# Kernel optimization log

Hardware: AMD Instinct MI355X
Metric: run time of the kernel (lower is better)

Reference implementation:

```python
import jax, jax.numpy as jnp
import numpy as np

N_NODES = 100000
N_EDGES = 1600000
D_IN = 64
D_HID = 64
D_OUT = 64


def _sage_conv(x, src, dst, n_nodes, W_l, b_l, W_r):
    # mean aggregation of source features at destination nodes
    msgs = x[src]  # [E, F] gather
    agg = jax.ops.segment_sum(msgs, dst, num_segments=n_nodes)
    cnt = jax.ops.segment_sum(jnp.ones((src.shape[0],), x.dtype), dst, num_segments=n_nodes)
    mean = agg / jnp.maximum(cnt, 1.0)[:, None]  # nodes with no in-edges -> 0
    # out = lin_l(mean) + lin_r(x); lin_l has bias, lin_r does not (PyG default)
    return mean @ W_l.T + b_l + x @ W_r.T


def setup_inputs() -> dict:
    key = jax.random.key(0)
    ks = jax.random.split(key, 8)
    x = jax.random.normal(ks[0], (N_NODES, D_IN), dtype=jnp.float32)
    edge_index = jax.random.randint(ks[1], (2, N_EDGES), 0, N_NODES, dtype=jnp.int64) if jax.config.jax_enable_x64 else jax.random.randint(ks[1], (2, N_EDGES), 0, N_NODES, dtype=jnp.int32)
    s1 = 1.0 / np.sqrt(D_IN)
    s2 = 1.0 / np.sqrt(D_HID)
    W1_l = jax.random.uniform(ks[2], (D_HID, D_IN), jnp.float32, -s1, s1)
    b1_l = jax.random.uniform(ks[3], (D_HID,), jnp.float32, -s1, s1)
    W1_r = jax.random.uniform(ks[4], (D_HID, D_IN), jnp.float32, -s1, s1)
    W2_l = jax.random.uniform(ks[5], (D_OUT, D_HID), jnp.float32, -s2, s2)
    b2_l = jax.random.uniform(ks[6], (D_OUT,), jnp.float32, -s2, s2)
    W2_r = jax.random.uniform(ks[7], (D_OUT, D_HID), jnp.float32, -s2, s2)
    return {"x": x, "edge_index": edge_index, "W1_l": W1_l, "b1_l": b1_l, "W1_r": W1_r,
            "W2_l": W2_l, "b2_l": b2_l, "W2_r": W2_r}


def reference(x, edge_index, W1_l, b1_l, W1_r, W2_l, b2_l, W2_r):
    src, dst = edge_index[0], edge_index[1]
    h = _sage_conv(x, src, dst, x.shape[0], W1_l, b1_l, W1_r)
    h = jax.nn.relu(h)
    out = _sage_conv(h, src, dst, x.shape[0], W2_l, b2_l, W2_r)
    return out
```

## Files before the change

### kernel.cpp

```cpp
#include <hip/hip_runtime.h>
#include <hip/hip_fp16.h>

#define N_NODES 100000
#define N_EDGES 1600000
#define D 64

#define BSHIFT 8
#define BUCK_N 256
#define NBUCK 391
#define EPB 4096
#define NBLKA 391
#define SCAN_N (NBUCK * NBLKA)
#define SCAN_B1 ((SCAN_N + 255) / 256)
#define A4_CAP 6144
#define X_OCTETS (N_NODES * D / 8)
#define NBIN 2048
#define CVT_BLKS ((X_OCTETS + 2048 + 511) / 512)

typedef _Float16 half8 __attribute__((ext_vector_type(8)));
typedef float floatx4 __attribute__((ext_vector_type(4)));


__device__ __forceinline__ uint4 pack8h(float4 a, float4 b) {
    __half2 h0, h1, h2, h3;
    h0.x = __float2half(a.x); h0.y = __float2half(a.y);
    h1.x = __float2half(a.z); h1.y = __float2half(a.w);
    h2.x = __float2half(b.x); h2.y = __float2half(b.y);
    h3.x = __float2half(b.z); h3.y = __float2half(b.w);
    uint4 pk;
    pk.x = *(unsigned int*)&h0; pk.y = *(unsigned int*)&h1;
    pk.z = *(unsigned int*)&h2; pk.w = *(unsigned int*)&h3;
    return pk;
}


__global__ void pre_k(const float* __restrict__ x,
                      const float* __restrict__ W1l, const float* __restrict__ W1r,
                      const float* __restrict__ W2l, const float* __restrict__ W2r,
                      const int* __restrict__ dst, int* __restrict__ histG,
                      __half* __restrict__ x16,
                      __half* __restrict__ o1l, __half* __restrict__ o1r,
                      __half* __restrict__ o2l, __half* __restrict__ o2r) {
    __shared__ int hl[512];
    int t = threadIdx.x;
    if (blockIdx.x < NBLKA) {
        hl[t] = 0;
        __syncthreads();
        int base = blockIdx.x * EPB;
#pragma unroll
        for (int r = 0; r < 8; r++) {
            int idx = base + r * 512 + t;
            if (idx < N_EDGES) atomicAdd(&hl[dst[idx] >> BSHIFT], 1);
        }
        __syncthreads();
        if (t < NBUCK) histG[t * NBLKA + blockIdx.x] = hl[t];
        return;
    }
    int i = (blockIdx.x - NBLKA) * 512 + t;
    const float* s;
    __half* d;
    int j;
    if (i < X_OCTETS) {
        s = x; d = x16; j = i * 8;
    } else {
        int k = i - X_OCTETS;
        if (k >= 2048) return;
        int arr = k >> 9;
        j = (k & 511) * 8;
        s = (arr == 0) ? W1l : (arr == 1) ? W1r : (arr == 2) ? W2l : W2r;
        d = (arr == 0) ? o1l : (arr == 1) ? o1r : (arr == 2) ? o2l : o2r;
    }
    float4 a = *(const float4*)&s[j];
    float4 b = *(const float4*)&s[j + 4];
    *(uint4*)&d[j] = pack8h(a, b);
}


__global__ void scan1_k(int* __restrict__ data, int* __restrict__ bsums, int n) {
    __shared__ int sm[256];
    int i = blockIdx.x * 256 + threadIdx.x;
    int v = (i < n) ? data[i] : 0;
    sm[threadIdx.x] = v;
    __syncthreads();
    for (int off = 1; off < 256; off <<= 1) {
        int t = (threadIdx.x >= off) ? sm[threadIdx.x - off] : 0;
        __syncthreads();
        sm[threadIdx.x] += t;
        __syncthreads();
    }
    if (i < n) data[i] = sm[threadIdx.x] - v;
    if (threadIdx.x == 255) bsums[blockIdx.x] = sm[255];
}

__global__ void scan2_k(int* __restrict__ bsums, int nb) {
    __shared__ int sm[1024];
    int v = (threadIdx.x < nb) ? bsums[threadIdx.x] : 0;
    sm[threadIdx.x] = v;
    __syncthreads();
    for (int off = 1; off < 1024; off <<= 1) {
        int t = (threadIdx.x >= off) ? sm[threadIdx.x - off] : 0;
        __syncthreads();
        sm[threadIdx.x] += t;
        __syncthreads();
    }
    if (threadIdx.x < nb) bsums[threadIdx.x] = sm[threadIdx.x];
}

__device__ __forceinline__ int hist_abs(const int* histG, const int* bsums, int idx) {
    int v = histG[idx];
    int blk = idx >> 8;
    if (blk > 0) v += bsums[blk - 1];
    return v;
}


__global__ void a3_sort_k(const int* __restrict__ src, const int* __restrict__ dst,
                          const int* __restrict__ histG, const int* __restrict__ bsums,
                          unsigned int* __restrict__ epacked, int e) {
    __shared__ int hl[512];
    __shared__ int cur[512];
    __shared__ int sc[512];
    __shared__ int gbase[NBUCK];
    __shared__ unsigned int spk[EPB];
    __shared__ unsigned short sb[EPB];
    int t = threadIdx.x;
    int blk = blockIdx.x;
    int base = blk * EPB;

    hl[t] = 0;
    __syncthreads();

    int myd[8], mys[8];
#pragma unroll
    for (int r = 0; r < 8; r++) {
        int idx = base + r * 512 + t;
        if (idx < e) {
            myd[r] = dst[idx];
            mys[r] = src[idx];
            atomicAdd(&hl[myd[r] >> BSHIFT], 1);
        } else {
            myd[r] = -1; mys[r] = 0;
        }
    }
    __syncthreads();

    int v = hl[t];
    sc[t] = v;
    __syncthreads();
    for (int off = 1; off < 512; off <<= 1) {
        int tt = (t >= off) ? sc[t - off] : 0;
        __syncthreads();
        sc[t] += tt;
        __syncthreads();
    }
    int excl = sc[t] - v;
    hl[t] = excl;
    cur[t] = excl;
    if (t < NBUCK) gbase[t] = hist_abs(histG, bsums, t * NBLKA + blk);
    __syncthreads();

#pragma unroll
    for (int r = 0; r < 8; r++) {
        if (myd[r] >= 0) {
            int b = myd[r] >> BSHIFT;
            int dl = myd[r] & (BUCK_N - 1);
            int pos = atomicAdd(&cur[b], 1);
            spk[pos] = ((unsigned)dl << 17) | (unsigned)mys[r];
            sb[pos] = (unsigned short)b;
        }
    }
    __syncthreads();

    int cnt = e - base; if (cnt > EPB) cnt = EPB;
#pragma unroll
    for (int r = 0; r < 8; r++) {
        int i = r * 512 + t;
        if (i < cnt) {
            int b = sb[i];
            epacked[gbase[b] + (i - hl[b])] = spk[i];
        }
    }
}


__global__ void a4_nodesort_k(unsigned int* __restrict__ epk,
                              const int* __restrict__ histG, const int* __restrict__ bsums,
                              int* __restrict__ row_ptr) {
    __shared__ int sorted[A4_CAP];
    __shared__ int hist[NBIN];
    __shared__ int cur[NBIN];
    __shared__ int sc[512];
    int b = blockIdx.x;
    int t = threadIdx.x;

    int s0 = hist_abs(histG, bsums, b * NBLKA);
    int s1 = (b == NBUCK - 1) ? N_EDGES : hist_abs(histG, bsums, (b + 1) * NBLKA);
    int cnt = s1 - s0;
    if (cnt > A4_CAP) cnt = A4_CAP;

#pragma unroll
    for (int i = 0; i < NBIN / 512; i++) hist[t + i * 512] = 0;
    __syncthreads();

    unsigned int my[12];
    int mycnt = 0;
    for (int i = t; i < cnt; i += 512) {
        unsigned int p = epk[s0 + i];
        my[mycnt++] = p;
        atomicAdd(&hist[((p >> 17) << 3) | ((p & 0x1FFFFu) >> 14)], 1);
    }
    __syncthreads();

    int b0 = t << 2;
    int h0 = hist[b0], h1 = hist[b0 + 1], h2 = hist[b0 + 2], h3 = hist[b0 + 3];
    int s = h0 + h1 + h2 + h3;
    sc[t] = s;
    __syncthreads();
    for (int off = 1; off < 512; off <<= 1) {
        int tt = (t >= off) ? sc[t - off] : 0;
        __syncthreads();
        sc[t] += tt;
        __syncthreads();
    }
    int base = sc[t] - s;
    cur[b0] = base;
    cur[b0 + 1] = base + h0;
    cur[b0 + 2] = base + h0 + h1;
    cur[b0 + 3] = base + h0 + h1 + h2;
    __syncthreads();

    if (t < 256) {
        int g = (b << BSHIFT) + t;
        if (g < N_NODES) row_ptr[g] = s0 + cur[t << 3];
    }
    __syncthreads();

    for (int i = 0; i < mycnt; i++) {
        unsigned int p = my[i];
        int pos = atomicAdd(&cur[((p >> 17) << 3) | ((p & 0x1FFFFu) >> 14)], 1);
        sorted[pos] = (int)(p & 0x1FFFF);
    }
    __syncthreads();

    for (int i = t; i < cnt; i += 512) epk[s0 + i] = (unsigned int)sorted[i];

    if (b == NBUCK - 1 && t == 0) row_ptr[N_NODES] = N_EDGES;
}


__device__ __forceinline__ void addp(__half2* a, uint4 v) {
    const __half2* h = (const __half2*)&v;
    a[0] = __hadd2(a[0], h[0]);
    a[1] = __hadd2(a[1], h[1]);
    a[2] = __hadd2(a[2], h[2]);
    a[3] = __hadd2(a[3], h[3]);
}

__global__ void agg9_k(const __half* __restrict__ feat16,
                       const int* __restrict__ row_ptr,
                       const int* __restrict__ adj,
                       __half* __restrict__ mean16, int n) {
    int t = threadIdx.x;
    int lane = t & 63;
    int w = t >> 6;
    int node = blockIdx.x * 32 + w * 8 + (lane >> 3);
    if (node >= n) return;
    int fp = lane & 7;
    int gl = lane & 56;
    const uint4* f16 = (const uint4*)feat16;

    int beg = row_ptr[node];
    int end = row_ptr[node + 1];
    __half2 z; z.x = __float2half(0.f); z.y = z.x;
    __half2 aA[4] = {z, z, z, z};
    __half2 aB[4] = {z, z, z, z};

    int e = beg;
    for (; e + 7 < end; e += 8) {
        int am = adj[e + fp];
        int n0 = __shfl(am, gl + 0);
        int n1 = __shfl(am, gl + 1);
        int n2 = __shfl(am, gl + 2);
        int n3 = __shfl(am, gl + 3);
        int n4 = __shfl(am, gl + 4);
        int n5 = __shfl(am, gl + 5);
        int n6 = __shfl(am, gl + 6);
        int n7 = __shfl(am, gl + 7);
        uint4 v0 = f16[(size_t)n0 * 8 + fp];
        uint4 v1 = f16[(size_t)n1 * 8 + fp];
        uint4 v2 = f16[(size_t)n2 * 8 + fp];
        uint4 v3 = f16[(size_t)n3 * 8 + fp];
        uint4 v4 = f16[(size_t)n4 * 8 + fp];
        uint4 v5 = f16[(size_t)n5 * 8 + fp];
        uint4 v6 = f16[(size_t)n6 * 8 + fp];
        uint4 v7 = f16[(size_t)n7 * 8 + fp];
        addp(aA, v0); addp(aB, v1); addp(aA, v2); addp(aB, v3);
        addp(aA, v4); addp(aB, v5); addp(aA, v6); addp(aB, v7);
    }
    if (e + 3 < end) {
        uint4 v0 = f16[(size_t)adj[e] * 8 + fp];
        uint4 v1 = f16[(size_t)adj[e + 1] * 8 + fp];
        uint4 v2 = f16[(size_t)adj[e + 2] * 8 + fp];
        uint4 v3 = f16[(size_t)adj[e + 3] * 8 + fp];
        addp(aA, v0); addp(aB, v1); addp(aA, v2); addp(aB, v3);
        e += 4;
    }
    for (; e < end; e++) addp(aA, f16[(size_t)adj[e] * 8 + fp]);

    int dg = end - beg;
    float inv = (dg > 1) ? 1.0f / (float)dg : 1.0f;
    float2 s0 = __half22float2(aA[0]), s1 = __half22float2(aA[1]);
    float2 s2 = __half22float2(aA[2]), s3 = __half22float2(aA[3]);
    float2 t0 = __half22float2(aB[0]), t1 = __half22float2(aB[1]);
    float2 t2 = __half22float2(aB[2]), t3 = __half22float2(aB[3]);
    float4 o0, o1;
    o0.x = (s0.x + t0.x) * inv; o0.y = (s0.y + t0.y) * inv;
    o0.z = (s1.x + t1.x) * inv; o0.w = (s1.y + t1.y) * inv;
    o1.x = (s2.x + t2.x) * inv; o1.y = (s2.y + t2.y) * inv;
    o1.z = (s3.x + t3.x) * inv; o1.w = (s3.y + t3.y) * inv;
    *(uint4*)&mean16[(size_t)node * D + 8 * fp] = pack8h(o0, o1);
}


#define NT 4

__global__ void gemm_mfma_k(const __half* __restrict__ Ap,
                            const __half* __restrict__ Fp,
                            const __half* __restrict__ Wl16,
                            const __half* __restrict__ Wr16,
                            const float* __restrict__ bl,
                            float* __restrict__ out32,
                            __half* __restrict__ out16,
                            int n, int do_relu) {
    int t = threadIdx.x;
    int wave = t >> 6;
    int lane = t & 63;
    int fcol = lane & 15;
    int quad = lane >> 4;
    int f = wave * 16 + fcol;

    half8 b0 = *(const half8*)(Wl16 + (size_t)f * 64 + quad * 8);
    half8 b1 = *(const half8*)(Wl16 + (size_t)f * 64 + 32 + quad * 8);
    half8 b2 = *(const half8*)(Wr16 + (size_t)f * 64 + quad * 8);
    half8 b3 = *(const half8*)(Wr16 + (size_t)f * 64 + 32 + quad * 8);
    float bias = bl[f];

    int ntiles = (n + 15) >> 4;
#pragma unroll
    for (int i = 0; i < NT; i++) {
        int tile = blockIdx.x * NT + i;
        if (tile >= ntiles) break;
        size_t arow = (size_t)(tile * 16 + fcol) * 64 + quad * 8;
        half8 a0 = *(const half8*)(Ap + arow);
        half8 a1 = *(const half8*)(Ap + arow + 32);
        half8 a2 = *(const half8*)(Fp + arow);
        half8 a3 = *(const half8*)(Fp + arow + 32);

        floatx4 acc = {0.f, 0.f, 0.f, 0.f};
        acc = __builtin_amdgcn_mfma_f32_16x16x32_f16(a0, b0, acc, 0, 0, 0);
        acc = __builtin_amdgcn_mfma_f32_16x16x32_f16(a1, b1, acc, 0, 0, 0);
        acc = __builtin_amdgcn_mfma_f32_16x16x32_f16(a2, b2, acc, 0, 0, 0);
        acc = __builtin_amdgcn_mfma_f32_16x16x32_f16(a3, b3, acc, 0, 0, 0);

#pragma unroll
        for (int r = 0; r < 4; r++) {
            int node = tile * 16 + quad * 4 + r;
            if (node >= n) break;
            float v = acc[r] + bias;
            if (do_relu) v = fmaxf(v, 0.f);
            if (out32) out32[(size_t)node * 64 + f] = v;
            if (out16) out16[(size_t)node * 64 + f] = __float2half(v);
        }
    }
}

extern "C" void kernel_launch(void* const* d_in, const int* in_sizes, int n_in,
                              void* d_out, int out_size, void* d_ws, size_t ws_size,
                              hipStream_t stream) {
    const float* x   = (const float*)d_in[0];
    const int*   ei  = (const int*)d_in[1];
    const float* W1l = (const float*)d_in[2];
    const float* b1l = (const float*)d_in[3];
    const float* W1r = (const float*)d_in[4];
    const float* W2l = (const float*)d_in[5];
    const float* b2l = (const float*)d_in[6];
    const float* W2r = (const float*)d_in[7];
    float* out = (float*)d_out;

    const int* src = ei;
    const int* dst = ei + N_EDGES;

    __half* agg16 = (__half*)d_ws;
    __half* x16   = agg16 + (size_t)N_NODES * D;
    __half* h16   = x16 + (size_t)N_NODES * D;
    __half* w1l16 = h16 + (size_t)N_NODES * D;
    __half* w1r16 = w1l16 + 4096;
    __half* w2l16 = w1r16 + 4096;
    __half* w2r16 = w2l16 + 4096;
    int*   histG = (int*)(w2r16 + 4096);
    int*   bsums = histG + SCAN_N;
    int*   row_ptr = bsums + 1024;
    unsigned int* epk = (unsigned int*)(row_ptr + N_NODES + 2);

    pre_k<<<NBLKA + CVT_BLKS, 512, 0, stream>>>(x, W1l, W1r, W2l, W2r, dst, histG,
                                                x16, w1l16, w1r16, w2l16, w2r16);

    scan1_k<<<SCAN_B1, 256, 0, stream>>>(histG, bsums, SCAN_N);
    scan2_k<<<1, 1024, 0, stream>>>(bsums, SCAN_B1);
    a3_sort_k<<<NBLKA, 512, 0, stream>>>(src, dst, histG, bsums, epk, N_EDGES);
    a4_nodesort_k<<<NBUCK, 512, 0, stream>>>(epk, histG, bsums, row_ptr);

    int ab = (N_NODES + 31) / 32;
    int gmb = ((N_NODES + 15) / 16 + NT - 1) / NT;

    agg9_k<<<ab, 256, 0, stream>>>(x16, row_ptr, (const int*)epk, agg16, N_NODES);
    gemm_mfma_k<<<gmb, 256, 0, stream>>>(agg16, x16, w1l16, w1r16, b1l,
                                         (float*)nullptr, h16, N_NODES, 1);
    agg9_k<<<ab, 256, 0, stream>>>(h16, row_ptr, (const int*)epk, agg16, N_NODES);
    gemm_mfma_k<<<gmb, 256, 0, stream>>>(agg16, h16, w2l16, w2r16, b2l,
                                         out, (__half*)nullptr, N_NODES, 0);
}
```

Before: 214.8 us.

## Fuse mean aggregation with MFMA linear layer and simplify node sort to 256 bins

Merges the gather-mean kernel and the MFMA GEMM into one kernel that keeps each block's 32-node mean tile in swizzled LDS. This removes the intermediate fp16 aggregate buffer writes and reads and two launches per forward. The per-bucket node sort now uses one bin per destination node instead of sub-binning by source range. That shortens the histogram and scan work, but it gives up the source-ordered adjacency that may have helped gather locality.

```diff
diff --git a/kernel.cpp b/kernel.cpp
--- a/kernel.cpp
+++ b/kernel.cpp
@@ -14,8 +14,8 @@
 #define SCAN_B1 ((SCAN_N + 255) / 256)
 #define A4_CAP 6144
 #define X_OCTETS (N_NODES * D / 8)
-#define NBIN 2048
 #define CVT_BLKS ((X_OCTETS + 2048 + 511) / 512)
+#define AGB (N_NODES / 32)
 
 typedef _Float16 half8 __attribute__((ext_vector_type(8)));
 typedef float floatx4 __attribute__((ext_vector_type(4)));
@@ -187,8 +187,8 @@
                               const int* __restrict__ histG, const int* __restrict__ bsums,
                               int* __restrict__ row_ptr) {
     __shared__ int sorted[A4_CAP];
-    __shared__ int hist[NBIN];
-    __shared__ int cur[NBIN];
+    __shared__ int hist[256];
+    __shared__ int cur[256];
     __shared__ int sc[512];
     int b = blockIdx.x;
     int t = threadIdx.x;
@@ -198,8 +198,7 @@
     int cnt = s1 - s0;
     if (cnt > A4_CAP) cnt = A4_CAP;
 
-#pragma unroll
-    for (int i = 0; i < NBIN / 512; i++) hist[t + i * 512] = 0;
+    if (t < 256) hist[t] = 0;
     __syncthreads();
 
     unsigned int my[12];
@@ -207,14 +206,12 @@
     for (int i = t; i < cnt; i += 512) {
         unsigned int p = epk[s0 + i];
         my[mycnt++] = p;
-        atomicAdd(&hist[((p >> 17) << 3) | ((p & 0x1FFFFu) >> 14)], 1);
-    }
-    __syncthreads();
-
-    int b0 = t << 2;
-    int h0 = hist[b0], h1 = hist[b0 + 1], h2 = hist[b0 + 2], h3 = hist[b0 + 3];
-    int s = h0 + h1 + h2 + h3;
-    sc[t] = s;
+        atomicAdd(&hist[p >> 17], 1);
+    }
+    __syncthreads();
+
+    int v = (t < 256) ? hist[t] : 0;
+    sc[t] = v;
     __syncthreads();
     for (int off = 1; off < 512; off <<= 1) {
         int tt = (t >= off) ? sc[t - off] : 0;
@@ -222,28 +219,23 @@
         sc[t] += tt;
         __syncthreads();
     }
-    int base = sc[t] - s;
-    cur[b0] = base;
-    cur[b0 + 1] = base + h0;
-    cur[b0 + 2] = base + h0 + h1;
-    cur[b0 + 3] = base + h0 + h1 + h2;
-    __syncthreads();
+    int start = sc[t] - v;
+    if (t < 256) cur[t] = start;
+    __syncthreads();
+
+    for (int i = 0; i < mycnt; i++) {
+        unsigned int p = my[i];
+        int pos = atomicAdd(&cur[p >> 17], 1);
+        sorted[pos] = (int)(p & 0x1FFFF);
+    }
+    __syncthreads();
+
+    for (int i = t; i < cnt; i += 512) epk[s0 + i] = (unsigned int)sorted[i];
 
     if (t < 256) {
         int g = (b << BSHIFT) + t;
-        if (g < N_NODES) row_ptr[g] = s0 + cur[t << 3];
-    }
-    __syncthreads();
-
-    for (int i = 0; i < mycnt; i++) {
-        unsigned int p = my[i];
-        int pos = atomicAdd(&cur[((p >> 17) << 3) | ((p & 0x1FFFFu) >> 14)], 1);
-        sorted[pos] = (int)(p & 0x1FFFF);
-    }
-    __syncthreads();
-
-    for (int i = t; i < cnt; i += 512) epk[s0 + i] = (unsigned int)sorted[i];
-
+        if (g < N_NODES) row_ptr[g] = s0 + start;
+    }
     if (b == NBUCK - 1 && t == 0) row_ptr[N_NODES] = N_EDGES;
 }
 
@@ -256,18 +248,33 @@
     a[3] = __hadd2(a[3], h[3]);
 }
 
-__global__ void agg9_k(const __half* __restrict__ feat16,
-                       const int* __restrict__ row_ptr,
-                       const int* __restrict__ adj,
-                       __half* __restrict__ mean16, int n) {
+__global__ void agg_gemm_k(const __half* __restrict__ feat16,
+                           const int* __restrict__ row_ptr,
+                           const int* __restrict__ adj,
+                           const __half* __restrict__ Wl16,
+                           const __half* __restrict__ Wr16,
+                           const float* __restrict__ bl,
+                           float* __restrict__ out32,
+                           __half* __restrict__ out16,
+                           int do_relu) {
+    __shared__ __half mt[32 * 64];
     int t = threadIdx.x;
     int lane = t & 63;
     int w = t >> 6;
-    int node = blockIdx.x * 32 + w * 8 + (lane >> 3);
-    if (node >= n) return;
     int fp = lane & 7;
     int gl = lane & 56;
+    int nloc = w * 8 + (lane >> 3);
+    int node = blockIdx.x * 32 + nloc;
     const uint4* f16 = (const uint4*)feat16;
+
+    int fcol = lane & 15;
+    int quad = lane >> 4;
+    int f = w * 16 + fcol;
+    half8 b0 = *(const half8*)(Wl16 + (size_t)f * 64 + quad * 8);
+    half8 b1 = *(const half8*)(Wl16 + (size_t)f * 64 + 32 + quad * 8);
+    half8 b2 = *(const half8*)(Wr16 + (size_t)f * 64 + quad * 8);
+    half8 b3 = *(const half8*)(Wr16 + (size_t)f * 64 + 32 + quad * 8);
+    float bias = bl[f];
 
     int beg = row_ptr[node];
     int end = row_ptr[node + 1];
@@ -318,43 +325,17 @@
     o0.z = (s1.x + t1.x) * inv; o0.w = (s1.y + t1.y) * inv;
     o1.x = (s2.x + t2.x) * inv; o1.y = (s2.y + t2.y) * inv;
     o1.z = (s3.x + t3.x) * inv; o1.w = (s3.y + t3.y) * inv;
-    *(uint4*)&mean16[(size_t)node * D + 8 * fp] = pack8h(o0, o1);
-}
-
-
-#define NT 4
-
-__global__ void gemm_mfma_k(const __half* __restrict__ Ap,
-                            const __half* __restrict__ Fp,
-                            const __half* __restrict__ Wl16,
-                            const __half* __restrict__ Wr16,
-                            const float* __restrict__ bl,
-                            float* __restrict__ out32,
-                            __half* __restrict__ out16,
-                            int n, int do_relu) {
-    int t = threadIdx.x;
-    int wave = t >> 6;
-    int lane = t & 63;
-    int fcol = lane & 15;
-    int quad = lane >> 4;
-    int f = wave * 16 + fcol;
-
-    half8 b0 = *(const half8*)(Wl16 + (size_t)f * 64 + quad * 8);
-    half8 b1 = *(const half8*)(Wl16 + (size_t)f * 64 + 32 + quad * 8);
-    half8 b2 = *(const half8*)(Wr16 + (size_t)f * 64 + quad * 8);
-    half8 b3 = *(const half8*)(Wr16 + (size_t)f * 64 + 32 + quad * 8);
-    float bias = bl[f];
-
-    int ntiles = (n + 15) >> 4;
-#pragma unroll
-    for (int i = 0; i < NT; i++) {
-        int tile = blockIdx.x * NT + i;
-        if (tile >= ntiles) break;
-        size_t arow = (size_t)(tile * 16 + fcol) * 64 + quad * 8;
-        half8 a0 = *(const half8*)(Ap + arow);
-        half8 a1 = *(const half8*)(Ap + arow + 32);
-        half8 a2 = *(const half8*)(Fp + arow);
-        half8 a3 = *(const half8*)(Fp + arow + 32);
+    *(uint4*)&mt[(size_t)nloc * 64 + 8 * (fp ^ (nloc & 7))] = pack8h(o0, o1);
+    __syncthreads();
+
+#pragma unroll
+    for (int tile = 0; tile < 2; tile++) {
+        int row = tile * 16 + fcol;
+        half8 a0 = *(const half8*)&mt[(size_t)row * 64 + 8 * (quad ^ (row & 7))];
+        half8 a1 = *(const half8*)&mt[(size_t)row * 64 + 8 * ((4 + quad) ^ (row & 7))];
+        size_t frow = ((size_t)blockIdx.x * 32 + row) * 64 + quad * 8;
+        half8 a2 = *(const half8*)(feat16 + frow);
+        half8 a3 = *(const half8*)(feat16 + frow + 32);
 
         floatx4 acc = {0.f, 0.f, 0.f, 0.f};
         acc = __builtin_amdgcn_mfma_f32_16x16x32_f16(a0, b0, acc, 0, 0, 0);
@@ -364,12 +345,11 @@
 
 #pragma unroll
         for (int r = 0; r < 4; r++) {
-            int node = tile * 16 + quad * 4 + r;
-            if (node >= n) break;
+            int node2 = blockIdx.x * 32 + tile * 16 + quad * 4 + r;
             float v = acc[r] + bias;
             if (do_relu) v = fmaxf(v, 0.f);
-            if (out32) out32[(size_t)node * 64 + f] = v;
-            if (out16) out16[(size_t)node * 64 + f] = __float2half(v);
+            if (out32) out32[(size_t)node2 * 64 + f] = v;
+            if (out16) out16[(size_t)node2 * 64 + f] = __float2half(v);
         }
     }
 }
@@ -390,8 +370,7 @@
     const int* src = ei;
     const int* dst = ei + N_EDGES;
 
-    __half* agg16 = (__half*)d_ws;
-    __half* x16   = agg16 + (size_t)N_NODES * D;
+    __half* x16   = (__half*)d_ws;
     __half* h16   = x16 + (size_t)N_NODES * D;
     __half* w1l16 = h16 + (size_t)N_NODES * D;
     __half* w1r16 = w1l16 + 4096;
@@ -410,13 +389,10 @@
     a3_sort_k<<<NBLKA, 512, 0, stream>>>(src, dst, histG, bsums, epk, N_EDGES);
     a4_nodesort_k<<<NBUCK, 512, 0, stream>>>(epk, histG, bsums, row_ptr);
 
-    int ab = (N_NODES + 31) / 32;
-    int gmb = ((N_NODES + 15) / 16 + NT - 1) / NT;
-
-    agg9_k<<<ab, 256, 0, stream>>>(x16, row_ptr, (const int*)epk, agg16, N_NODES);
-    gemm_mfma_k<<<gmb, 256, 0, stream>>>(agg16, x16, w1l16, w1r16, b1l,
-                                         (float*)nullptr, h16, N_NODES, 1);
-    agg9_k<<<ab, 256, 0, stream>>>(h16, row_ptr, (const int*)epk, agg16, N_NODES);
-    gemm_mfma_k<<<gmb, 256, 0, stream>>>(agg16, h16, w2l16, w2r16, b2l,
-                                         out, (__half*)nullptr, N_NODES, 0);
-}
+    agg_gemm_k<<<AGB, 256, 0, stream>>>(x16, row_ptr, (const int*)epk,
+                                        w1l16, w1r16, b1l,
+                                        (float*)nullptr, h16, 1);
+    agg_gemm_k<<<AGB, 256, 0, stream>>>(h16, row_ptr, (const int*)epk,
+                                        w2l16, w2r16, b2l,
+                                        out, (__half*)nullptr, 0);
+}
```

Measured after the change: 196.9 us, median of 2. 8.3% less time.
